# Optimization experiments

Measured on AMD Instinct MI355X. Metric: run time of the kernel, lower is better.

The kernel has to match this reference:

```python
import jax, jax.numpy as jnp
import numpy as np

N = 100000      # nodes
E = 1600000     # edges
G = 256         # graphs
DF = 64         # dim_feature
DH = 64         # dim_h
DM = 3 * DH     # transformer d_model = 192
NH = 8          # heads
HD = DM // NH   # head dim = 24
FF = 2048       # torch TransformerEncoderLayer default dim_feedforward
EPS_BN = 1e-5
EPS_LN = 1e-5


def setup_inputs() -> dict:
    key = jax.random.key(0)
    ks = iter(jax.random.split(key, 64))
    def rn(shape, scale=0.05):
        return jax.random.normal(next(ks), shape, dtype=jnp.float32) * scale
    inp = {}
    inp["x"] = jax.random.normal(next(ks), (N, DF), dtype=jnp.float32)
    inp["edge_index"] = jax.random.randint(next(ks), (2, E), 0, N, dtype=jnp.int64)
    inp["batch"] = jnp.sort(jax.random.randint(next(ks), (N,), 0, G, dtype=jnp.int64))
    # GIN nn1: Linear(DF,DH) + BN(DH) + ReLU + Linear(DH,DH) + ReLU
    for p, din in (("nn1", DF), ("nn2", DH)):
        inp[f"{p}_w1"] = rn((DH, din)); inp[f"{p}_b1"] = rn((DH,))
        inp[f"{p}_bn_g"] = 1.0 + rn((DH,)); inp[f"{p}_bn_b"] = rn((DH,))
        inp[f"{p}_bn_m"] = rn((DH,)); inp[f"{p}_bn_v"] = 0.5 + jax.random.uniform(next(ks), (DH,), dtype=jnp.float32)
        inp[f"{p}_w2"] = rn((DH, DH)); inp[f"{p}_b2"] = rn((DH,))
    # Transformer encoder layer (post-LN, relu, eval mode)
    inp["qkv_w"] = rn((3 * DM, DM)); inp["qkv_b"] = rn((3 * DM,))
    inp["attn_out_w"] = rn((DM, DM)); inp["attn_out_b"] = rn((DM,))
    inp["ln1_g"] = 1.0 + rn((DM,)); inp["ln1_b"] = rn((DM,))
    inp["ff1_w"] = rn((FF, DM)); inp["ff1_b"] = rn((FF,))
    inp["ff2_w"] = rn((DM, FF)); inp["ff2_b"] = rn((DM,))
    inp["ln2_g"] = 1.0 + rn((DM,)); inp["ln2_b"] = rn((DM,))
    # Head
    inp["lin1_w"] = rn((DM, DM)); inp["lin1_b"] = rn((DM,))
    inp["lin2_w"] = rn((1, DM)); inp["lin2_b"] = rn((1,))
    return inp


def _mlp(h, w1, b1, g, b, m, v, w2, b2):
    # Linear -> BatchNorm1d (eval) -> ReLU -> Linear -> ReLU
    h = h @ w1.T + b1
    h = g * (h - m) * jax.lax.rsqrt(v + EPS_BN) + b
    h = jax.nn.relu(h)
    return jax.nn.relu(h @ w2.T + b2)


def _gin(h, src, dst, params):
    # GINConv eps=0: nn(x + sum-aggregated neighbor messages)
    agg = jax.ops.segment_sum(h[src], dst, num_segments=N)
    return _mlp(h + agg, *params)


def _layernorm(h, g, b):
    mu = jnp.mean(h, axis=-1, keepdims=True)
    var = jnp.mean(jnp.square(h - mu), axis=-1, keepdims=True)
    return (h - mu) * jax.lax.rsqrt(var + EPS_LN) * g + b


def reference(x, edge_index, batch,
              nn1_w1, nn1_b1, nn1_bn_g, nn1_bn_b, nn1_bn_m, nn1_bn_v, nn1_w2, nn1_b2,
              nn2_w1, nn2_b1, nn2_bn_g, nn2_bn_b, nn2_bn_m, nn2_bn_v, nn2_w2, nn2_b2,
              qkv_w, qkv_b, attn_out_w, attn_out_b, ln1_g, ln1_b,
              ff1_w, ff1_b, ff2_w, ff2_b, ln2_g, ln2_b,
              lin1_w, lin1_b, lin2_w, lin2_b):
    src, dst = edge_index[0], edge_index[1]
    p1 = (nn1_w1, nn1_b1, nn1_bn_g, nn1_bn_b, nn1_bn_m, nn1_bn_v, nn1_w2, nn1_b2)
    p2 = (nn2_w1, nn2_b1, nn2_bn_g, nn2_bn_b, nn2_bn_m, nn2_bn_v, nn2_w2, nn2_b2)
    h1 = jax.nn.relu(_gin(x, src, dst, p1))
    h2 = jax.nn.relu(_gin(h1, src, dst, p2))
    h3 = jax.nn.relu(_gin(h2, src, dst, p2))  # conv3 shares nn2 weights
    # global_add_pool each layer, concat -> [G, 3*DH]
    h = jnp.concatenate([jax.ops.segment_sum(hh, batch, num_segments=G) for hh in (h1, h2, h3)], axis=1)
    h = h[:, None, :]  # [G, 1, DM] (seq_len = 1)
    # Self-attention (post-LN encoder layer, eval mode)
    qkv = h @ qkv_w.T + qkv_b                      # [G,1,3*DM]
    q, k, v = jnp.split(qkv, 3, axis=-1)
    def heads(t):
        return t.reshape(G, 1, NH, HD).transpose(0, 2, 1, 3)  # [G,NH,1,HD]
    q, k, v = heads(q), heads(k), heads(v)
    scores = jnp.einsum('ghqd,ghkd->ghqk', q, k) / np.sqrt(HD).astype(np.float32)
    attn = jnp.einsum('ghqk,ghkd->ghqd', jax.nn.softmax(scores, axis=-1), v)
    attn = attn.transpose(0, 2, 1, 3).reshape(G, 1, DM) @ attn_out_w.T + attn_out_b
    h = _layernorm(h + attn, ln1_g, ln1_b)
    ff = jax.nn.relu(h @ ff1_w.T + ff1_b) @ ff2_w.T + ff2_b
    h = _layernorm(h + ff, ln2_g, ln2_b)
    h = jnp.mean(h, axis=1)                        # [G, DM]
    h = jax.nn.relu(h @ lin1_w.T + lin1_b)         # dropout is identity in eval
    return h @ lin2_w.T + lin2_b                   # [G, 1]
```

## Files before the change

kernel.cpp:

```cpp
#include <hip/hip_runtime.h>

#define NNODES 100000
#define NGRAPH 256
#define DHID 64
#define DMODEL 192
#define DFF 2048
#define SCAN_CHUNK 512
#define NCH ((NNODES + SCAN_CHUNK - 1) / SCAN_CHUNK)

__global__ __launch_bounds__(256) void hist_kernel(
    const int* __restrict__ dstv, int* __restrict__ cnt, int E)
{
    for (int e = blockIdx.x * blockDim.x + threadIdx.x; e < E;
         e += gridDim.x * blockDim.x)
        atomicAdd(&cnt[dstv[e]], 1);
}

__global__ __launch_bounds__(SCAN_CHUNK) void scan_chunk_kernel(
    const int* __restrict__ cnt, int* __restrict__ excl,
    int* __restrict__ tot, int n)
{
    __shared__ int buf[SCAN_CHUNK];
    int i = blockIdx.x * SCAN_CHUNK + threadIdx.x;
    int v = (i < n) ? cnt[i] : 0;
    buf[threadIdx.x] = v;
    __syncthreads();
    for (int off = 1; off < SCAN_CHUNK; off <<= 1) {
        int t = (threadIdx.x >= off) ? buf[threadIdx.x - off] : 0;
        __syncthreads();
        buf[threadIdx.x] += t;
        __syncthreads();
    }
    if (i < n) excl[i] = buf[threadIdx.x] - v;
    if (threadIdx.x == SCAN_CHUNK - 1) tot[blockIdx.x] = buf[threadIdx.x];
}

__global__ __launch_bounds__(256) void scan_tot_kernel(int* __restrict__ tot, int nch)
{
    __shared__ int buf[256];
    int v = (threadIdx.x < nch) ? tot[threadIdx.x] : 0;
    buf[threadIdx.x] = v;
    __syncthreads();
    for (int off = 1; off < 256; off <<= 1) {
        int t = (threadIdx.x >= off) ? buf[threadIdx.x - off] : 0;
        __syncthreads();
        buf[threadIdx.x] += t;
        __syncthreads();
    }
    if (threadIdx.x < nch) tot[threadIdx.x] = buf[threadIdx.x] - v;
}

__global__ __launch_bounds__(256) void finalize_rowptr_kernel(
    const int* __restrict__ excl, const int* __restrict__ tot,
    int* __restrict__ rowptr, int* __restrict__ cursor, int n, int E)
{
    for (int i = blockIdx.x * blockDim.x + threadIdx.x; i <= n;
         i += gridDim.x * blockDim.x) {
        if (i < n) {
            int v = excl[i] + tot[i / SCAN_CHUNK];
            rowptr[i] = v;
            cursor[i] = v;
        } else {
            rowptr[n] = E;
        }
    }
}

__global__ __launch_bounds__(256) void sort_edges_kernel(
    const int* __restrict__ srcv, const int* __restrict__ dstv,
    int* __restrict__ cursor, int* __restrict__ out, int E)
{
    for (int e = blockIdx.x * blockDim.x + threadIdx.x; e < E;
         e += gridDim.x * blockDim.x) {
        int p = atomicAdd(&cursor[dstv[e]], 1);
        out[p] = srcv[e];
    }
}

__global__ __launch_bounds__(256) void gin_fused_kernel(
    const float* __restrict__ hin,
    const int* __restrict__ rowptr, const int* __restrict__ srcs,
    const float* __restrict__ w1, const float* __restrict__ b1,
    const float* __restrict__ bng, const float* __restrict__ bnb,
    const float* __restrict__ bnm, const float* __restrict__ bnv,
    const float* __restrict__ w2, const float* __restrict__ b2,
    float* __restrict__ hout, float* __restrict__ pool,
    const int* __restrict__ batch)
{
    __shared__ float w1s[DHID][DHID + 1];
    __shared__ float w2s[DHID][DHID + 1];
    __shared__ float tbuf[4][DHID];

    int tid = threadIdx.x;
    for (int idx = tid; idx < DHID * DHID; idx += 256) {
        int j = idx >> 6, k = idx & 63;
        w1s[j][k] = w1[idx];
        w2s[j][k] = w2[idx];
    }
    __syncthreads();

    int lane = tid & 63;
    int w    = tid >> 6;

    float rs  = rsqrtf(bnv[lane] + 1e-5f);
    float sc  = bng[lane] * rs;
    float sh  = bnb[lane] - bnm[lane] * sc;
    float bb1 = b1[lane];
    float bb2 = b2[lane];

    int wid    = blockIdx.x * 4 + w;
    int nwaves = gridDim.x * 4;
    int per    = (NNODES + nwaves - 1) / nwaves;
    int n0     = wid * per;
    int n1     = min(n0 + per, NNODES);
    if (n0 >= n1) return;

    float poolacc = 0.0f;
    int   curg    = batch[n0];

    for (int n = n0; n < n1; ++n) {
        float acc = hin[n * DHID + lane];
        int jb = rowptr[n], je = rowptr[n + 1];
        int j  = jb;
        for (; j + 3 < je; j += 4) {
            int s0 = srcs[j], s1 = srcs[j + 1], s2 = srcs[j + 2], s3 = srcs[j + 3];
            float a0 = hin[s0 * DHID + lane];
            float a1 = hin[s1 * DHID + lane];
            float a2 = hin[s2 * DHID + lane];
            float a3 = hin[s3 * DHID + lane];
            acc += (a0 + a1) + (a2 + a3);
        }
        for (; j < je; ++j) acc += hin[srcs[j] * DHID + lane];

        tbuf[w][lane] = acc;
        float y = bb1;
        #pragma unroll
        for (int k = 0; k < DHID; ++k) y += tbuf[w][k] * w1s[lane][k];
        y = fmaxf(y * sc + sh, 0.0f);
        tbuf[w][lane] = y;
        float z = bb2;
        #pragma unroll
        for (int k = 0; k < DHID; ++k) z += tbuf[w][k] * w2s[lane][k];
        z = fmaxf(z, 0.0f);

        if (hout) hout[n * DHID + lane] = z;

        int g = batch[n];
        if (g != curg) {
            atomicAdd(&pool[curg * DHID + lane], poolacc);
            poolacc = 0.0f;
            curg = g;
        }
        poolacc += z;
    }
    atomicAdd(&pool[curg * DHID + lane], poolacc);
}

__global__ __launch_bounds__(192) void head_kernel(
    const float* __restrict__ pools,
    const float* __restrict__ qkv_w, const float* __restrict__ qkv_b,
    const float* __restrict__ aow,   const float* __restrict__ aob,
    const float* __restrict__ ln1g,  const float* __restrict__ ln1b,
    const float* __restrict__ ff1w,  const float* __restrict__ ff1b,
    const float* __restrict__ ff2w,  const float* __restrict__ ff2b,
    const float* __restrict__ ln2g,  const float* __restrict__ ln2b,
    const float* __restrict__ l1w,   const float* __restrict__ l1b,
    const float* __restrict__ l2w,   const float* __restrict__ l2b,
    float* __restrict__ out)
{
    __shared__ float A[DMODEL], B[DMODEL], C[DMODEL];
    __shared__ float ffb[DFF];
    __shared__ float red[DMODEL];

    int g = blockIdx.x, tid = threadIdx.x;

    A[tid] = pools[(tid >> 6) * (NGRAPH * DHID) + g * DHID + (tid & 63)];
    __syncthreads();

    {
        float acc = qkv_b[384 + tid];
        const float* wr = qkv_w + (384 + tid) * DMODEL;
        for (int k = 0; k < DMODEL; ++k) acc += A[k] * wr[k];
        B[tid] = acc;
    }
    __syncthreads();

    {
        float acc = aob[tid];
        const float* wr = aow + tid * DMODEL;
        for (int k = 0; k < DMODEL; ++k) acc += B[k] * wr[k];
        C[tid] = A[tid] + acc;
    }
    __syncthreads();

    {
        float mu = 0.0f;
        for (int k = 0; k < DMODEL; ++k) mu += C[k];
        mu *= (1.0f / DMODEL);
        float var = 0.0f;
        for (int k = 0; k < DMODEL; ++k) { float d = C[k] - mu; var += d * d; }
        var *= (1.0f / DMODEL);
        float rstd = rsqrtf(var + 1e-5f);
        B[tid] = (C[tid] - mu) * rstd * ln1g[tid] + ln1b[tid];
    }
    __syncthreads();

    for (int o = tid; o < DFF; o += DMODEL) {
        float acc = ff1b[o];
        const float* wr = ff1w + o * DMODEL;
        for (int k = 0; k < DMODEL; ++k) acc += B[k] * wr[k];
        ffb[o] = fmaxf(acc, 0.0f);
    }
    __syncthreads();

    {
        float acc = ff2b[tid];
        const float* wr = ff2w + tid * DFF;
        for (int k = 0; k < DFF; ++k) acc += ffb[k] * wr[k];
        C[tid] = B[tid] + acc;
    }
    __syncthreads();

    {
        float mu = 0.0f;
        for (int k = 0; k < DMODEL; ++k) mu += C[k];
        mu *= (1.0f / DMODEL);
        float var = 0.0f;
        for (int k = 0; k < DMODEL; ++k) { float d = C[k] - mu; var += d * d; }
        var *= (1.0f / DMODEL);
        float rstd = rsqrtf(var + 1e-5f);
        A[tid] = (C[tid] - mu) * rstd * ln2g[tid] + ln2b[tid];
    }
    __syncthreads();

    {
        float acc = l1b[tid];
        const float* wr = l1w + tid * DMODEL;
        for (int k = 0; k < DMODEL; ++k) acc += A[k] * wr[k];
        B[tid] = fmaxf(acc, 0.0f);
    }
    __syncthreads();

    red[tid] = B[tid] * l2w[tid];
    __syncthreads();
    if (tid == 0) {
        float s = 0.0f;
        for (int k = 0; k < DMODEL; ++k) s += red[k];
        out[g] = s + l2b[0];
    }
}

extern "C" void kernel_launch(void* const* d_in, const int* in_sizes, int n_in,
                              void* d_out, int out_size, void* d_ws, size_t ws_size,
                              hipStream_t stream)
{
    const float* x    = (const float*)d_in[0];
    const int*   ei   = (const int*)d_in[1];
    const int*   bat  = (const int*)d_in[2];
    const int    E    = in_sizes[1] / 2;
    const int*   src  = ei;
    const int*   dst  = ei + E;

    const float* nn1[8]; for (int i = 0; i < 8; ++i) nn1[i] = (const float*)d_in[3 + i];
    const float* nn2[8]; for (int i = 0; i < 8; ++i) nn2[i] = (const float*)d_in[11 + i];
    const float* qkv_w = (const float*)d_in[19];
    const float* qkv_b = (const float*)d_in[20];
    const float* aow   = (const float*)d_in[21];
    const float* aob   = (const float*)d_in[22];
    const float* ln1g  = (const float*)d_in[23];
    const float* ln1b  = (const float*)d_in[24];
    const float* ff1w  = (const float*)d_in[25];
    const float* ff1b  = (const float*)d_in[26];
    const float* ff2w  = (const float*)d_in[27];
    const float* ff2b  = (const float*)d_in[28];
    const float* ln2g  = (const float*)d_in[29];
    const float* ln2b  = (const float*)d_in[30];
    const float* l1w   = (const float*)d_in[31];
    const float* l1b   = (const float*)d_in[32];
    const float* l2w   = (const float*)d_in[33];
    const float* l2b   = (const float*)d_in[34];

    const size_t N64 = (size_t)NNODES * DHID;

    float* h1    = (float*)d_ws;
    float* h2    = h1 + N64;
    float* pools = h2 + N64;
    int*   cnt    = (int*)(pools + 3 * NGRAPH * DHID);
    int*   excl   = cnt + NNODES;
    int*   rowptr = excl + NNODES;
    int*   cursor = rowptr + NNODES + 1;
    int*   tot    = cursor + NNODES;
    int*   srcs   = tot + NCH + 4;

    hipMemsetAsync(cnt, 0, NNODES * sizeof(int), stream);
    hipMemsetAsync(pools, 0, 3 * NGRAPH * DHID * sizeof(float), stream);
    hist_kernel<<<1024, 256, 0, stream>>>(dst, cnt, E);
    scan_chunk_kernel<<<NCH, SCAN_CHUNK, 0, stream>>>(cnt, excl, tot, NNODES);
    scan_tot_kernel<<<1, 256, 0, stream>>>(tot, NCH);
    finalize_rowptr_kernel<<<128, 256, 0, stream>>>(excl, tot, rowptr, cursor, NNODES, E);
    sort_edges_kernel<<<1024, 256, 0, stream>>>(src, dst, cursor, srcs, E);

    const int LB = 1024;

    gin_fused_kernel<<<LB, 256, 0, stream>>>(x, rowptr, srcs,
        nn1[0], nn1[1], nn1[2], nn1[3], nn1[4], nn1[5], nn1[6], nn1[7],
        h1, pools + 0 * NGRAPH * DHID, bat);

    gin_fused_kernel<<<LB, 256, 0, stream>>>(h1, rowptr, srcs,
        nn2[0], nn2[1], nn2[2], nn2[3], nn2[4], nn2[5], nn2[6], nn2[7],
        h2, pools + 1 * NGRAPH * DHID, bat);

    gin_fused_kernel<<<LB, 256, 0, stream>>>(h2, rowptr, srcs,
        nn2[0], nn2[1], nn2[2], nn2[3], nn2[4], nn2[5], nn2[6], nn2[7],
        nullptr, pools + 2 * NGRAPH * DHID, bat);

    head_kernel<<<NGRAPH, DMODEL, 0, stream>>>(pools,
        qkv_w, qkv_b, aow, aob, ln1g, ln1b,
        ff1w, ff1b, ff2w, ff2b, ln2g, ln2b,
        l1w, l1b, l2w, l2b, (float*)d_out);
}
```

Measured before the change: 719.5 us.

## Split transformer head into batched kernels with transposed weights, register GIN weights

Replaces the single per-graph head kernel with three kernels. They use transposed weight copies so weight reads are coalesced, and they batch several graphs per block so each FF weight load is reused. The transpose runs on every call. The GIN kernel now keeps each lane's weight row in registers instead of shared memory, reads tbuf as float4, and unrolls the neighbour gather 8-wide. Grid sizes for the histogram and sort kernels are doubled. Costs include extra launches, workspace traffic for the transposed weights and intermediates, and higher register pressure in the GIN kernel.

```diff
diff --git a/kernel.cpp b/kernel.cpp
--- a/kernel.cpp
+++ b/kernel.cpp
@@ -74,6 +74,38 @@
          e += gridDim.x * blockDim.x) {
         int p = atomicAdd(&cursor[dstv[e]], 1);
         out[p] = srcv[e];
+    }
+}
+
+__global__ __launch_bounds__(256) void transpose_w_kernel(
+    const float* __restrict__ qkv_w, const float* __restrict__ aow,
+    const float* __restrict__ l1w,  const float* __restrict__ ff1w,
+    const float* __restrict__ ff2w,
+    float* __restrict__ vwT, float* __restrict__ aowT, float* __restrict__ l1T,
+    float* __restrict__ f1T, float* __restrict__ f2T)
+{
+    const int S1 = DMODEL * DMODEL;
+    const int S2 = DMODEL * DFF;
+    int total = 3 * S1 + 2 * S2;
+    for (int idx = blockIdx.x * blockDim.x + threadIdx.x; idx < total;
+         idx += gridDim.x * blockDim.x) {
+        if (idx < 3 * S1) {
+            int a = idx / S1, r = idx % S1;
+            int k = r / DMODEL, o = r % DMODEL;
+            if (a == 0)      vwT[r]  = qkv_w[(2 * DMODEL + o) * DMODEL + k];
+            else if (a == 1) aowT[r] = aow[o * DMODEL + k];
+            else             l1T[r]  = l1w[o * DMODEL + k];
+        } else {
+            int r = idx - 3 * S1;
+            if (r < S2) {
+                int k = r >> 11, o = r & (DFF - 1);
+                f1T[r] = ff1w[o * DMODEL + k];
+            } else {
+                r -= S2;
+                int k = r / DMODEL, o = r % DMODEL;
+                f2T[r] = ff2w[o * DFF + k];
+            }
+        }
     }
 }
 
@@ -87,20 +119,20 @@
     float* __restrict__ hout, float* __restrict__ pool,
     const int* __restrict__ batch)
 {
-    __shared__ float w1s[DHID][DHID + 1];
-    __shared__ float w2s[DHID][DHID + 1];
-    __shared__ float tbuf[4][DHID];
-
-    int tid = threadIdx.x;
-    for (int idx = tid; idx < DHID * DHID; idx += 256) {
-        int j = idx >> 6, k = idx & 63;
-        w1s[j][k] = w1[idx];
-        w2s[j][k] = w2[idx];
-    }
-    __syncthreads();
-
+    __shared__ float tbuf[4][68];
+
+    int tid  = threadIdx.x;
     int lane = tid & 63;
     int w    = tid >> 6;
+
+    float W1[DHID], W2[DHID];
+    #pragma unroll
+    for (int k = 0; k < DHID; k += 4) {
+        float4 a = *(const float4*)&w1[lane * DHID + k];
+        W1[k] = a.x; W1[k+1] = a.y; W1[k+2] = a.z; W1[k+3] = a.w;
+        float4 b = *(const float4*)&w2[lane * DHID + k];
+        W2[k] = b.x; W2[k+1] = b.y; W2[k+2] = b.z; W2[k+3] = b.w;
+    }
 
     float rs  = rsqrtf(bnv[lane] + 1e-5f);
     float sc  = bng[lane] * rs;
@@ -122,25 +154,37 @@
         float acc = hin[n * DHID + lane];
         int jb = rowptr[n], je = rowptr[n + 1];
         int j  = jb;
-        for (; j + 3 < je; j += 4) {
-            int s0 = srcs[j], s1 = srcs[j + 1], s2 = srcs[j + 2], s3 = srcs[j + 3];
+        for (; j + 7 < je; j += 8) {
+            int s0 = srcs[j],     s1 = srcs[j + 1], s2 = srcs[j + 2], s3 = srcs[j + 3];
+            int s4 = srcs[j + 4], s5 = srcs[j + 5], s6 = srcs[j + 6], s7 = srcs[j + 7];
             float a0 = hin[s0 * DHID + lane];
             float a1 = hin[s1 * DHID + lane];
             float a2 = hin[s2 * DHID + lane];
             float a3 = hin[s3 * DHID + lane];
-            acc += (a0 + a1) + (a2 + a3);
+            float a4 = hin[s4 * DHID + lane];
+            float a5 = hin[s5 * DHID + lane];
+            float a6 = hin[s6 * DHID + lane];
+            float a7 = hin[s7 * DHID + lane];
+            acc += ((a0 + a1) + (a2 + a3)) + ((a4 + a5) + (a6 + a7));
         }
         for (; j < je; ++j) acc += hin[srcs[j] * DHID + lane];
 
         tbuf[w][lane] = acc;
         float y = bb1;
         #pragma unroll
-        for (int k = 0; k < DHID; ++k) y += tbuf[w][k] * w1s[lane][k];
+        for (int k = 0; k < DHID; k += 4) {
+            float4 t4 = *(const float4*)&tbuf[w][k];
+            y += t4.x * W1[k] + t4.y * W1[k+1] + t4.z * W1[k+2] + t4.w * W1[k+3];
+        }
         y = fmaxf(y * sc + sh, 0.0f);
+
         tbuf[w][lane] = y;
         float z = bb2;
         #pragma unroll
-        for (int k = 0; k < DHID; ++k) z += tbuf[w][k] * w2s[lane][k];
+        for (int k = 0; k < DHID; k += 4) {
+            float4 t4 = *(const float4*)&tbuf[w][k];
+            z += t4.x * W2[k] + t4.y * W2[k+1] + t4.z * W2[k+2] + t4.w * W2[k+3];
+        }
         z = fmaxf(z, 0.0f);
 
         if (hout) hout[n * DHID + lane] = z;
@@ -156,97 +200,178 @@
     atomicAdd(&pool[curg * DHID + lane], poolacc);
 }
 
-__global__ __launch_bounds__(192) void head_kernel(
-    const float* __restrict__ pools,
-    const float* __restrict__ qkv_w, const float* __restrict__ qkv_b,
-    const float* __restrict__ aow,   const float* __restrict__ aob,
-    const float* __restrict__ ln1g,  const float* __restrict__ ln1b,
-    const float* __restrict__ ff1w,  const float* __restrict__ ff1b,
-    const float* __restrict__ ff2w,  const float* __restrict__ ff2b,
-    const float* __restrict__ ln2g,  const float* __restrict__ ln2b,
-    const float* __restrict__ l1w,   const float* __restrict__ l1b,
-    const float* __restrict__ l2w,   const float* __restrict__ l2b,
+__global__ __launch_bounds__(192) void head_a_kernel(
+    const float* __restrict__ pools, const float* __restrict__ vwT,
+    const float* __restrict__ qkv_b, const float* __restrict__ aowT,
+    const float* __restrict__ aob,   const float* __restrict__ ln1g,
+    const float* __restrict__ ln1b,  float* __restrict__ Bln)
+{
+    __shared__ float As[DMODEL], Vs[DMODEL], Cs[DMODEL];
+    int g = blockIdx.x, tid = threadIdx.x;
+
+    As[tid] = pools[(tid >> 6) * (NGRAPH * DHID) + g * DHID + (tid & 63)];
+    __syncthreads();
+
+    float acc = qkv_b[2 * DMODEL + tid];
+    #pragma unroll 8
+    for (int k = 0; k < DMODEL; ++k) acc += As[k] * vwT[k * DMODEL + tid];
+    Vs[tid] = acc;
+    __syncthreads();
+
+    acc = aob[tid];
+    #pragma unroll 8
+    for (int k = 0; k < DMODEL; ++k) acc += Vs[k] * aowT[k * DMODEL + tid];
+    float c = As[tid] + acc;
+    Cs[tid] = c;
+    __syncthreads();
+
+    float mu = 0.0f;
+    #pragma unroll
+    for (int k = 0; k < DMODEL; k += 4) {
+        float4 q = *(const float4*)&Cs[k];
+        mu += (q.x + q.y) + (q.z + q.w);
+    }
+    mu *= (1.0f / DMODEL);
+    float var = 0.0f;
+    #pragma unroll
+    for (int k = 0; k < DMODEL; k += 4) {
+        float4 q = *(const float4*)&Cs[k];
+        float d0 = q.x - mu, d1 = q.y - mu, d2 = q.z - mu, d3 = q.w - mu;
+        var += (d0 * d0 + d1 * d1) + (d2 * d2 + d3 * d3);
+    }
+    var *= (1.0f / DMODEL);
+    float rstd = rsqrtf(var + 1e-5f);
+    Bln[g * DMODEL + tid] = (c - mu) * rstd * ln1g[tid] + ln1b[tid];
+}
+
+__global__ __launch_bounds__(256) void head_ff1_kernel(
+    const float* __restrict__ Bln, const float* __restrict__ f1T,
+    const float* __restrict__ ff1b, float* __restrict__ ffb)
+{
+    __shared__ float Bs[8][DMODEL];
+    int bo = blockIdx.x & 7, bg = blockIdx.x >> 3;
+    int tid = threadIdx.x;
+    int o = bo * 256 + tid;
+
+    for (int idx = tid; idx < 8 * DMODEL; idx += 256)
+        Bs[idx / DMODEL][idx % DMODEL] = Bln[(bg * 8 + idx / DMODEL) * DMODEL + idx % DMODEL];
+    __syncthreads();
+
+    float acc[8];
+    #pragma unroll
+    for (int gi = 0; gi < 8; ++gi) acc[gi] = 0.0f;
+    float bias = ff1b[o];
+
+    #pragma unroll 2
+    for (int k = 0; k < DMODEL; k += 4) {
+        float w0 = f1T[k * DFF + o];
+        float w1 = f1T[(k + 1) * DFF + o];
+        float w2 = f1T[(k + 2) * DFF + o];
+        float w3 = f1T[(k + 3) * DFF + o];
+        #pragma unroll
+        for (int gi = 0; gi < 8; ++gi) {
+            float4 b4 = *(const float4*)&Bs[gi][k];
+            acc[gi] += b4.x * w0 + b4.y * w1 + b4.z * w2 + b4.w * w3;
+        }
+    }
+    #pragma unroll
+    for (int gi = 0; gi < 8; ++gi)
+        ffb[(bg * 8 + gi) * DFF + o] = fmaxf(acc[gi] + bias, 0.0f);
+}
+
+__global__ __launch_bounds__(384) void head_ff2_kernel(
+    const float* __restrict__ ffb,  const float* __restrict__ f2T,
+    const float* __restrict__ ff2b, const float* __restrict__ Bln,
+    const float* __restrict__ ln2g, const float* __restrict__ ln2b,
+    const float* __restrict__ l1T,  const float* __restrict__ l1b,
+    const float* __restrict__ l2w,  const float* __restrict__ l2b,
     float* __restrict__ out)
 {
-    __shared__ float A[DMODEL], B[DMODEL], C[DMODEL];
-    __shared__ float ffb[DFF];
-    __shared__ float red[DMODEL];
-
-    int g = blockIdx.x, tid = threadIdx.x;
-
-    A[tid] = pools[(tid >> 6) * (NGRAPH * DHID) + g * DHID + (tid & 63)];
-    __syncthreads();
-
-    {
-        float acc = qkv_b[384 + tid];
-        const float* wr = qkv_w + (384 + tid) * DMODEL;
-        for (int k = 0; k < DMODEL; ++k) acc += A[k] * wr[k];
-        B[tid] = acc;
-    }
-    __syncthreads();
-
-    {
-        float acc = aob[tid];
-        const float* wr = aow + tid * DMODEL;
-        for (int k = 0; k < DMODEL; ++k) acc += B[k] * wr[k];
-        C[tid] = A[tid] + acc;
-    }
-    __syncthreads();
-
-    {
-        float mu = 0.0f;
-        for (int k = 0; k < DMODEL; ++k) mu += C[k];
-        mu *= (1.0f / DMODEL);
-        float var = 0.0f;
-        for (int k = 0; k < DMODEL; ++k) { float d = C[k] - mu; var += d * d; }
-        var *= (1.0f / DMODEL);
-        float rstd = rsqrtf(var + 1e-5f);
-        B[tid] = (C[tid] - mu) * rstd * ln1g[tid] + ln1b[tid];
-    }
-    __syncthreads();
-
-    for (int o = tid; o < DFF; o += DMODEL) {
-        float acc = ff1b[o];
-        const float* wr = ff1w + o * DMODEL;
-        for (int k = 0; k < DMODEL; ++k) acc += B[k] * wr[k];
-        ffb[o] = fmaxf(acc, 0.0f);
-    }
-    __syncthreads();
-
-    {
-        float acc = ff2b[tid];
-        const float* wr = ff2w + tid * DFF;
-        for (int k = 0; k < DFF; ++k) acc += ffb[k] * wr[k];
-        C[tid] = B[tid] + acc;
-    }
-    __syncthreads();
-
-    {
-        float mu = 0.0f;
-        for (int k = 0; k < DMODEL; ++k) mu += C[k];
-        mu *= (1.0f / DMODEL);
-        float var = 0.0f;
-        for (int k = 0; k < DMODEL; ++k) { float d = C[k] - mu; var += d * d; }
-        var *= (1.0f / DMODEL);
-        float rstd = rsqrtf(var + 1e-5f);
-        A[tid] = (C[tid] - mu) * rstd * ln2g[tid] + ln2b[tid];
-    }
-    __syncthreads();
-
-    {
-        float acc = l1b[tid];
-        const float* wr = l1w + tid * DMODEL;
-        for (int k = 0; k < DMODEL; ++k) acc += A[k] * wr[k];
-        B[tid] = fmaxf(acc, 0.0f);
-    }
-    __syncthreads();
-
-    red[tid] = B[tid] * l2w[tid];
-    __syncthreads();
-    if (tid == 0) {
+    __shared__ float ffs[2][DFF];
+    __shared__ float ps[2][2][DMODEL];
+    __shared__ float Cs[2][DMODEL], As2[2][DMODEL], Bs2[2][DMODEL];
+
+    int g0 = blockIdx.x * 2, tid = threadIdx.x;
+
+    for (int idx = tid; idx < 2 * DFF; idx += 384)
+        ffs[idx >> 11][idx & (DFF - 1)] = ffb[g0 * DFF + idx];
+    __syncthreads();
+
+    int o  = (tid < DMODEL) ? tid : tid - DMODEL;
+    int kh = (tid < DMODEL) ? 0 : 1;
+    float acc0 = 0.0f, acc1 = 0.0f;
+    int kb = kh * (DFF / 2);
+    #pragma unroll 2
+    for (int k = kb; k < kb + DFF / 2; k += 4) {
+        float w0 = f2T[k * DMODEL + o];
+        float w1 = f2T[(k + 1) * DMODEL + o];
+        float w2 = f2T[(k + 2) * DMODEL + o];
+        float w3 = f2T[(k + 3) * DMODEL + o];
+        float4 q0 = *(const float4*)&ffs[0][k];
+        float4 q1 = *(const float4*)&ffs[1][k];
+        acc0 += q0.x * w0 + q0.y * w1 + q0.z * w2 + q0.w * w3;
+        acc1 += q1.x * w0 + q1.y * w1 + q1.z * w2 + q1.w * w3;
+    }
+    ps[kh][0][o] = acc0;
+    ps[kh][1][o] = acc1;
+    __syncthreads();
+
+    if (tid < DMODEL) {
+        #pragma unroll
+        for (int gi = 0; gi < 2; ++gi)
+            Cs[gi][tid] = ff2b[tid] + ps[0][gi][tid] + ps[1][gi][tid]
+                        + Bln[(g0 + gi) * DMODEL + tid];
+    }
+    __syncthreads();
+
+    if (tid < DMODEL) {
+        #pragma unroll
+        for (int gi = 0; gi < 2; ++gi) {
+            float mu = 0.0f;
+            #pragma unroll
+            for (int k = 0; k < DMODEL; k += 4) {
+                float4 q = *(const float4*)&Cs[gi][k];
+                mu += (q.x + q.y) + (q.z + q.w);
+            }
+            mu *= (1.0f / DMODEL);
+            float var = 0.0f;
+            #pragma unroll
+            for (int k = 0; k < DMODEL; k += 4) {
+                float4 q = *(const float4*)&Cs[gi][k];
+                float d0 = q.x - mu, d1 = q.y - mu, d2 = q.z - mu, d3 = q.w - mu;
+                var += (d0 * d0 + d1 * d1) + (d2 * d2 + d3 * d3);
+            }
+            var *= (1.0f / DMODEL);
+            float rstd = rsqrtf(var + 1e-5f);
+            As2[gi][tid] = (Cs[gi][tid] - mu) * rstd * ln2g[tid] + ln2b[tid];
+        }
+    }
+    __syncthreads();
+
+    if (tid < DMODEL) {
+        #pragma unroll
+        for (int gi = 0; gi < 2; ++gi) {
+            float acc = l1b[tid];
+            #pragma unroll 4
+            for (int k = 0; k < DMODEL; k += 4) {
+                float4 a4 = *(const float4*)&As2[gi][k];
+                acc += a4.x * l1T[k * DMODEL + tid] + a4.y * l1T[(k + 1) * DMODEL + tid]
+                     + a4.z * l1T[(k + 2) * DMODEL + tid] + a4.w * l1T[(k + 3) * DMODEL + tid];
+            }
+            Bs2[gi][tid] = fmaxf(acc, 0.0f);
+        }
+    }
+    __syncthreads();
+
+    if (tid < 2) {
         float s = 0.0f;
-        for (int k = 0; k < DMODEL; ++k) s += red[k];
-        out[g] = s + l2b[0];
+        #pragma unroll
+        for (int k = 0; k < DMODEL; k += 4) {
+            float4 b4 = *(const float4*)&Bs2[tid][k];
+            float4 w4 = *(const float4*)&l2w[k];
+            s += (b4.x * w4.x + b4.y * w4.y) + (b4.z * w4.z + b4.w * w4.w);
+        }
+        out[g0 + tid] = s + l2b[0];
     }
 }
 
@@ -281,11 +406,20 @@
     const float* l2b   = (const float*)d_in[34];
 
     const size_t N64 = (size_t)NNODES * DHID;
+    const int S1 = DMODEL * DMODEL;
+    const int S2 = DMODEL * DFF;
 
     float* h1    = (float*)d_ws;
     float* h2    = h1 + N64;
     float* pools = h2 + N64;
-    int*   cnt    = (int*)(pools + 3 * NGRAPH * DHID);
+    float* Bln   = pools + 3 * NGRAPH * DHID;
+    float* ffb   = Bln + NGRAPH * DMODEL;
+    float* vwT   = ffb + NGRAPH * DFF;
+    float* aowT  = vwT + S1;
+    float* l1T   = aowT + S1;
+    float* f1T   = l1T + S1;
+    float* f2T   = f1T + S2;
+    int*   cnt    = (int*)(f2T + S2);
     int*   excl   = cnt + NNODES;
     int*   rowptr = excl + NNODES;
     int*   cursor = rowptr + NNODES + 1;
@@ -294,11 +428,13 @@
 
     hipMemsetAsync(cnt, 0, NNODES * sizeof(int), stream);
     hipMemsetAsync(pools, 0, 3 * NGRAPH * DHID * sizeof(float), stream);
-    hist_kernel<<<1024, 256, 0, stream>>>(dst, cnt, E);
+    hist_kernel<<<2048, 256, 0, stream>>>(dst, cnt, E);
     scan_chunk_kernel<<<NCH, SCAN_CHUNK, 0, stream>>>(cnt, excl, tot, NNODES);
     scan_tot_kernel<<<1, 256, 0, stream>>>(tot, NCH);
     finalize_rowptr_kernel<<<128, 256, 0, stream>>>(excl, tot, rowptr, cursor, NNODES, E);
-    sort_edges_kernel<<<1024, 256, 0, stream>>>(src, dst, cursor, srcs, E);
+    sort_edges_kernel<<<2048, 256, 0, stream>>>(src, dst, cursor, srcs, E);
+    transpose_w_kernel<<<1024, 256, 0, stream>>>(qkv_w, aow, l1w, ff1w, ff2w,
+                                                 vwT, aowT, l1T, f1T, f2T);
 
     const int LB = 1024;
 
@@ -314,8 +450,9 @@
         nn2[0], nn2[1], nn2[2], nn2[3], nn2[4], nn2[5], nn2[6], nn2[7],
         nullptr, pools + 2 * NGRAPH * DHID, bat);
 
-    head_kernel<<<NGRAPH, DMODEL, 0, stream>>>(pools,
-        qkv_w, qkv_b, aow, aob, ln1g, ln1b,
-        ff1w, ff1b, ff2w, ff2b, ln2g, ln2b,
-        l1w, l1b, l2w, l2b, (float*)d_out);
-}
+    head_a_kernel<<<NGRAPH, DMODEL, 0, stream>>>(pools, vwT, qkv_b, aowT, aob,
+                                                 ln1g, ln1b, Bln);
+    head_ff1_kernel<<<256, 256, 0, stream>>>(Bln, f1T, ff1b, ffb);
+    head_ff2_kernel<<<NGRAPH / 2, 384, 0, stream>>>(ffb, f2T, ff2b, Bln,
+        ln2g, ln2b, l1T, l1b, l2w, l2b, (float*)d_out);
+}
```

Measured after the change: 975.9 us. 1.36x slower.
